# Optimization experiments

Measured on AMD Instinct MI355X. Metric: run time of the kernel, lower is better.

## Reference

```python
import jax, jax.numpy as jnp
import numpy as np

NUM_HEADS = 16
EMBED_DIM = 1024
HEAD_DIM = EMBED_DIM // NUM_HEADS


def _rel_shift(r):
    # r: (B, tlen, rlen). Pad with ONES (faithful to original), shift, tril.
    B, tlen, rlen = r.shape
    pad = jnp.ones((B, tlen, 1), dtype=r.dtype)
    rp = jnp.concatenate([pad, r], axis=2).reshape(B, rlen + 1, tlen)
    return jnp.tril(rp[:, 1:, :].reshape(B, tlen, rlen))


def setup_inputs() -> dict:
    key = jax.random.key(0)
    ks = jax.random.split(key, 12)
    T, B, E, H, D = 128, 8, EMBED_DIM, NUM_HEADS, HEAD_DIM
    query = jax.random.normal(ks[0], (T, B, E), dtype=jnp.float32)
    key_t = jax.random.normal(ks[1], (T, B, E), dtype=jnp.float32)
    value = jax.random.normal(ks[2], (T, B, E), dtype=jnp.float32)
    rel_pe = jax.random.normal(ks[3], (T, B, E), dtype=jnp.float32)
    # causal mask: True = masked (future positions)
    causal = ~jnp.tril(jnp.ones((T, T), dtype=bool))
    attn_mask = jnp.broadcast_to(causal, (B * H, T, T))
    utt_mask = jnp.ones((B * H, T, T, 1), dtype=jnp.float32)
    spk_mask = jax.random.randint(ks[4], (B, T, T), 0, 2, dtype=jnp.int32)
    s = 1.0 / np.sqrt(E)
    q_w = jax.random.uniform(ks[5], (E, E), jnp.float32, -s, s)
    k_w = jax.random.uniform(ks[6], (E, E), jnp.float32, -s, s)
    v_w = jax.random.uniform(ks[7], (E, E), jnp.float32, -s, s)
    r_w = jax.random.uniform(ks[8], (E, E), jnp.float32, -s, s)
    spk_emb = jax.random.uniform(ks[9], (2, E), jnp.float32, -s, s)
    out_w = jax.random.uniform(ks[10], (E, E), jnp.float32, -s, s)
    return {"query": query, "key": key_t, "value": value, "rel_pe": rel_pe,
            "attn_mask": attn_mask, "utt_mask": utt_mask, "spk_mask": spk_mask,
            "q_w": q_w, "k_w": k_w, "v_w": v_w, "r_w": r_w,
            "spk_emb": spk_emb, "out_w": out_w}


def reference(query, key, value, rel_pe, attn_mask, utt_mask, spk_mask,
              q_w, k_w, v_w, r_w, spk_emb, out_w):
    T, B, E = query.shape
    H, D = NUM_HEADS, HEAD_DIM
    scaling = float(D) ** -0.5

    def split_heads(x):  # (T, B, E) -> (B*H, T, D)
        return x.reshape(T, B * H, D).transpose(1, 0, 2)

    # NOTE: original computes k and v from `query` (faithful)
    q = split_heads(query @ q_w.T)
    k = split_heads(query @ k_w.T)
    v = split_heads(query @ v_w.T)
    r = split_heads(rel_pe @ r_w.T)

    # s_q: speaker embedding row 0 broadcast to all positions
    s_q = split_heads(jnp.broadcast_to(spk_emb[0], (T, B, E)))
    # s_k: (B, T, T, E) -> (B*H, T, T, D), same reshape chain as original
    s_k = spk_emb[spk_mask]                                   # (B, T, T, E)
    s_k = s_k.reshape(B, T * T, E).transpose(1, 0, 2)         # (T*T, B, E)
    s_k = s_k.reshape(T * T, B * H, D).transpose(1, 0, 2)     # (B*H, T*T, D)
    s_k = s_k.reshape(B * H, T, T, D) * utt_mask              # (B*H, T, T, D)

    new_q = q + s_q
    a1 = jnp.einsum('nid,njd->nij', new_q, k)
    a2 = jnp.einsum('nid,nijd->nij', new_q, s_k)
    a3 = _rel_shift(jnp.einsum('nid,njd->nij', s_q, r))

    w = (a1 + a2 + a3) * scaling
    w = jnp.where(attn_mask, jnp.asarray(1e-30, w.dtype), w)
    w = jax.nn.softmax(w, axis=-1)

    out = jnp.einsum('nij,njd->nid', w, v)                    # (B*H, T, D)
    out = out.transpose(1, 0, 2).reshape(T, B, E) @ out_w.T
    return out
```

## Files before the change

### kernel.cpp

```cpp
#include <hip/hip_runtime.h>
#include <hip/hip_bf16.h>
#include <cstddef>
#include <cstdint>


typedef _Float16 f16;
typedef __attribute__((ext_vector_type(8))) _Float16 f16x8;
typedef __attribute__((ext_vector_type(4))) float f32x4;

#define GLOBAL_TO_LDS(g, l) __builtin_amdgcn_global_load_lds( \
    (const __attribute__((address_space(1))) void*)(g),       \
    (__attribute__((address_space(3))) void*)(l), 16, 0, 0)

#define PIPE_SYNC(N) do {                                      \
    asm volatile("s_waitcnt vmcnt(" #N ")" ::: "memory");      \
    __builtin_amdgcn_s_barrier();                              \
    __builtin_amdgcn_sched_barrier(0);                         \
} while (0)

struct Ptr7 { const float* s[7]; };

__global__ __launch_bounds__(256) void tof16_kernel(Ptr7 p, f16* dbase)
{
    const float* s = p.s[blockIdx.y];
    f16* d = dbase + (size_t)blockIdx.y * (1u << 20);
    const int i = (blockIdx.x * 256 + threadIdx.x) * 8;
    const float4 a = *(const float4*)(s + i);
    const float4 b = *(const float4*)(s + i + 4);
    f16x8 o;
    o[0] = (f16)a.x; o[1] = (f16)a.y; o[2] = (f16)a.z; o[3] = (f16)a.w;
    o[4] = (f16)b.x; o[5] = (f16)b.y; o[6] = (f16)b.z; o[7] = (f16)b.w;
    *(f16x8*)(d + i) = o;
}

template <int TM, int TN>
__device__ __forceinline__ void gemm3ph_acc(const f16* __restrict__ A,
                                            const f16* __restrict__ B,
                                            int m0, int n0,
                                            f32x4 (&acc)[TM / 32][TN / 32])
{
    constexpr int AITS = TM / 32, BITS = TN / 32;
    constexpr int LD = AITS + BITS;
    constexpr int FM = TM / 32, FN = TN / 32;
    __shared__ __attribute__((aligned(16))) f16 As0[TM * 64];
    __shared__ __attribute__((aligned(16))) f16 As1[TM * 64];
    __shared__ __attribute__((aligned(16))) f16 As2[TM * 64];
    __shared__ __attribute__((aligned(16))) f16 Bs0[TN * 64];
    __shared__ __attribute__((aligned(16))) f16 Bs1[TN * 64];
    __shared__ __attribute__((aligned(16))) f16 Bs2[TN * 64];
    const int tid = threadIdx.x;
    const int wave = tid >> 6, lane = tid & 63;
    const int wr = wave >> 1, wc = wave & 1;
    const int l16 = lane & 15, lk = lane >> 4;

    auto stage = [&](f16* as_, f16* bs_, int k0) {
#pragma unroll
        for (int it = 0; it < AITS; ++it) {
            const int ebase = it * 2048 + wave * 512;
            const int e = ebase + lane * 8;
            const int row = e >> 6, slot = (e >> 3) & 7;
            const int scol = (slot ^ (row & 7)) << 3;
            GLOBAL_TO_LDS(A + (size_t)(m0 + row) * 1024 + k0 + scol, as_ + ebase);
        }
#pragma unroll
        for (int it = 0; it < BITS; ++it) {
            const int ebase = it * 2048 + wave * 512;
            const int e = ebase + lane * 8;
            const int row = e >> 6, slot = (e >> 3) & 7;
            const int scol = (slot ^ (row & 7)) << 3;
            GLOBAL_TO_LDS(B + (size_t)(n0 + row) * 1024 + k0 + scol, bs_ + ebase);
        }
    };
    auto compute = [&](const f16* as_, const f16* bs_) {
#pragma unroll
        for (int ksl = 0; ksl < 2; ++ksl) {
            const int s = ksl * 4 + lk;
            f16x8 af[FM], bg[FN];
#pragma unroll
            for (int mi = 0; mi < FM; ++mi) {
                const int r = wr * (TM / 2) + mi * 16 + l16;
                af[mi] = *(const f16x8*)(as_ + r * 64 + ((s ^ (r & 7)) << 3));
            }
#pragma unroll
            for (int ni = 0; ni < FN; ++ni) {
                const int r = wc * (TN / 2) + ni * 16 + l16;
                bg[ni] = *(const f16x8*)(bs_ + r * 64 + ((s ^ (r & 7)) << 3));
            }
            __builtin_amdgcn_s_setprio(1);
#pragma unroll
            for (int mi = 0; mi < FM; ++mi)
#pragma unroll
                for (int ni = 0; ni < FN; ++ni)
                    acc[mi][ni] = __builtin_amdgcn_mfma_f32_16x16x32_f16(
                        af[mi], bg[ni], acc[mi][ni], 0, 0, 0);
            __builtin_amdgcn_s_setprio(0);
        }
    };
    auto sync_steady = [&]() {
        if constexpr (LD == 6) PIPE_SYNC(6);
        else if constexpr (LD == 5) PIPE_SYNC(5);
        else PIPE_SYNC(4);
    };

    stage(As0, Bs0, 0);
    stage(As1, Bs1, 64);
    int k = 0;
#pragma unroll 1
    for (int t = 0; t < 15; t += 3) {
        sync_steady();
        if (t + 2 < 16) stage(As2, Bs2, k + 128);
        compute(As0, Bs0);
        sync_steady();
        if (t + 3 < 16) stage(As0, Bs0, k + 192);
        compute(As1, Bs1);
        sync_steady();
        if (t + 4 < 16) stage(As1, Bs1, k + 256);
        compute(As2, Bs2);
        k += 192;
    }
    PIPE_SYNC(0);
    compute(As0, Bs0);
}

__global__ __launch_bounds__(256) void proj4_kernel(
    const f16* __restrict__ qf, const f16* __restrict__ rf,
    const f16* __restrict__ wbase, const float* __restrict__ spk_emb,
    f16* __restrict__ Qh, f16* __restrict__ Kh, f16* __restrict__ VhT,
    float* __restrict__ CB, float* __restrict__ DD)
{
    const int bid = blockIdx.x;
    const int z = (bid & 7) >> 1;
    const int w = ((bid >> 3) << 1) | (bid & 1);
    const int m0 = (w >> 3) << 6;
    const int n0 = (w & 7) << 7;
    const f16* A = (z == 3) ? rf : qf;
    const f16* W = wbase + ((size_t)z << 20);

    f32x4 acc[2][4] = {};
    gemm3ph_acc<64, 128>(A, W, m0, n0, acc);

    const int tid = threadIdx.x;
    const int wave = tid >> 6, lane = tid & 63;
    const int wr = wave >> 1, wc = wave & 1;
    const int l16 = lane & 15, lk = lane >> 4;
    const int h = (n0 >> 6) + wc;

    if (z == 0) {
        float s0v[4], s1v[4];
#pragma unroll
        for (int ni = 0; ni < 4; ++ni) {
            const int c = (h << 6) + ni * 16 + l16;
            s0v[ni] = spk_emb[c];
            s1v[ni] = spk_emb[1024 + c];
        }
#pragma unroll
        for (int mi = 0; mi < 2; ++mi)
#pragma unroll
            for (int r = 0; r < 4; ++r) {
                const int row = m0 + wr * 32 + mi * 16 + lk * 4 + r;
                const int b = row & 7, t = row >> 3;
                float p0 = 0.f, p1 = 0.f;
#pragma unroll
                for (int ni = 0; ni < 4; ++ni) {
                    const float x = acc[mi][ni][r] + s0v[ni];
                    const int d = ni * 16 + l16;
                    Qh[(size_t)(((b << 4) + h) * 128 + t) * 64 + d] = (f16)x;
                    p0 = fmaf(x, s0v[ni], p0);
                    p1 = fmaf(x, s1v[ni], p1);
                }
#pragma unroll
                for (int off = 1; off < 16; off <<= 1) {
                    p0 += __shfl_xor(p0, off, 64);
                    p1 += __shfl_xor(p1, off, 64);
                }
                if (l16 == 0) {
                    const int n = (b << 4) + h;
                    DD[n * 128 + t] = p0;
                    DD[16384 + n * 128 + t] = p1;
                }
            }
    } else if (z == 3) {
        float s0v[4];
#pragma unroll
        for (int ni = 0; ni < 4; ++ni)
            s0v[ni] = spk_emb[(h << 6) + ni * 16 + l16];
#pragma unroll
        for (int mi = 0; mi < 2; ++mi)
#pragma unroll
            for (int r = 0; r < 4; ++r) {
                const int row = m0 + wr * 32 + mi * 16 + lk * 4 + r;
                const int b = row & 7, j = row >> 3;
                float p = 0.f;
#pragma unroll
                for (int ni = 0; ni < 4; ++ni)
                    p = fmaf(acc[mi][ni][r], s0v[ni], p);
#pragma unroll
                for (int off = 1; off < 16; off <<= 1)
                    p += __shfl_xor(p, off, 64);
                if (l16 == 0)
                    CB[((b << 4) + h) * 128 + j] = p;
            }
    } else {
        f16* dst = (z == 1) ? Kh : VhT;
#pragma unroll
        for (int mi = 0; mi < 2; ++mi)
#pragma unroll
            for (int r = 0; r < 4; ++r) {
                const int row = m0 + wr * 32 + mi * 16 + lk * 4 + r;
                const int b = row & 7, t = row >> 3;
#pragma unroll
                for (int ni = 0; ni < 4; ++ni) {
                    const int d = ni * 16 + l16;
                    const f16 x = (f16)acc[mi][ni][r];
                    if (z == 1)
                        dst[(size_t)(((b << 4) + h) * 128 + t) * 64 + d] = x;
                    else
                        dst[(size_t)(((b << 4) + h) * 64 + d) * 128 + t] = x;
                }
            }
    }
}

__global__ __launch_bounds__(256) void out_kernel(
    const f16* __restrict__ ATT, const f16* __restrict__ owf,
    float* __restrict__ out)
{
    const int bid = blockIdx.x;
    const int m0 = (bid >> 4) << 6;
    const int n0 = (bid & 15) << 6;
    f32x4 acc[2][2] = {};
    gemm3ph_acc<64, 64>(ATT, owf, m0, n0, acc);
    const int tid = threadIdx.x;
    const int wave = tid >> 6, lane = tid & 63;
    const int wr = wave >> 1, wc = wave & 1;
    const int l16 = lane & 15, lk = lane >> 4;
#pragma unroll
    for (int mi = 0; mi < 2; ++mi)
#pragma unroll
        for (int ni = 0; ni < 2; ++ni)
#pragma unroll
            for (int r = 0; r < 4; ++r) {
                const int row = m0 + wr * 32 + mi * 16 + lk * 4 + r;
                const int col = n0 + wc * 32 + ni * 16 + l16;
                out[(size_t)row * 1024 + col] = acc[mi][ni][r];
            }
}

__global__ __launch_bounds__(256) void attn_mfma_kernel(
    const f16* __restrict__ Qh, const f16* __restrict__ Kh,
    const f16* __restrict__ VhT,
    const float* __restrict__ CB, const float* __restrict__ DD,
    const int* __restrict__ spk_mask, const float* __restrict__ utt_mask,
    f16* __restrict__ ATT)
{
    __shared__ __attribute__((aligned(16))) char smem[58368];
    f16* nq = (f16*)smem;
    f16* kt = (f16*)(smem + 8192);
    f16* vt = (f16*)(smem + 24576);
    f16* psb = (f16*)(smem + 40960);
    float* cbuf = (float*)(smem + 57344);
    float* ddl  = (float*)(smem + 57856);

    const int bx = blockIdx.x, n = bx >> 1, half = bx & 1;
    const int b = n >> 4, h = n & 15, i0 = half << 6;
    const int tid = threadIdx.x, wave = tid >> 6, lane = tid & 63;
    const int l16 = lane & 15, lk = lane >> 4;
    const int il0 = wave * 16 + lk * 4;
    const size_t hb = (size_t)n * (128 * 64);

#pragma unroll
    for (int it = 0; it < 2; ++it) {
        const int ebase = it * 2048 + wave * 512;
        const int e = ebase + lane * 8;
        const int row = e >> 6, slot = (e >> 3) & 7;
        const int scol = (slot ^ (row & 7)) << 3;
        GLOBAL_TO_LDS(Qh + hb + (size_t)(i0 + row) * 64 + scol, nq + ebase);
    }
#pragma unroll
    for (int it = 0; it < 4; ++it) {
        const int ebase = it * 2048 + wave * 512;
        const int e = ebase + lane * 8;
        const int row = e >> 6, slot = (e >> 3) & 7;
        const int scol = (slot ^ (row & 7)) << 3;
        GLOBAL_TO_LDS(Kh + hb + (size_t)row * 64 + scol, kt + ebase);
    }
#pragma unroll
    for (int it = 0; it < 4; ++it) {
        const int ebase = it * 2048 + wave * 512;
        const int e = ebase + lane * 8;
        const int row = e >> 7, slot = (e >> 3) & 15;
        const int scol = (slot ^ (row & 7)) << 3;
        GLOBAL_TO_LDS(VhT + hb + (size_t)row * 128 + scol, vt + ebase);
    }

    if (tid < 128) {
        cbuf[tid] = CB[n * 128 + tid];
    } else {
        const int t2 = tid - 128;
        ddl[t2] = DD[(t2 >> 6) * 16384 + n * 128 + i0 + (t2 & 63)];
    }

    float du[8][4];
    int   sm[8][4];
#pragma unroll
    for (int ni = 0; ni < 8; ++ni) {
        const int j = ni * 16 + l16;
#pragma unroll
        for (int r = 0; r < 4; ++r) {
            const int i = i0 + il0 + r;
            du[ni][r] = utt_mask[((size_t)n * 128 + i) * 128 + j];
            sm[ni][r] = spk_mask[((size_t)b * 128 + i) * 128 + j];
        }
    }
    __syncthreads();

    const int iw = wave * 16 + l16;
    f16x8 af[2];
#pragma unroll
    for (int ksl = 0; ksl < 2; ++ksl) {
        const int s = ksl * 4 + lk;
        af[ksl] = *(const f16x8*)(nq + iw * 64 + ((s ^ (iw & 7)) << 3));
    }
    f32x4 sacc[8] = {};
#pragma unroll
    for (int ksl = 0; ksl < 2; ++ksl) {
        const int s = ksl * 4 + lk;
#pragma unroll
        for (int ni = 0; ni < 8; ++ni) {
            const int j = ni * 16 + l16;
            const f16x8 bg = *(const f16x8*)(kt + j * 64 + ((s ^ (j & 7)) << 3));
            sacc[ni] = __builtin_amdgcn_mfma_f32_16x16x32_f16(af[ksl], bg, sacc[ni], 0, 0, 0);
        }
    }

    float sc[8][4];
#pragma unroll
    for (int ni = 0; ni < 8; ++ni) {
        const int j = ni * 16 + l16;
#pragma unroll
        for (int r = 0; r < 4; ++r) {
            const int il = il0 + r, i = i0 + il;
            const float a2 = du[ni][r] * (sm[ni][r] ? ddl[64 + il] : ddl[il]);
            const float a3 = (j <= i) ? cbuf[127 - i + j] : 0.f;
            const float v = (sacc[ni][r] + a2 + a3) * 0.125f;
            sc[ni][r] = (j > i) ? 1e-30f : v;
        }
    }
    float inv[4];
    f16* ps = psb + wave * 2048;
#pragma unroll
    for (int r = 0; r < 4; ++r) {
        float m = sc[0][r];
#pragma unroll
        for (int ni = 1; ni < 8; ++ni) m = fmaxf(m, sc[ni][r]);
#pragma unroll
        for (int off = 8; off > 0; off >>= 1) m = fmaxf(m, __shfl_xor(m, off, 64));
        float ssum = 0.f;
#pragma unroll
        for (int ni = 0; ni < 8; ++ni) {
            const float e = __expf(sc[ni][r] - m);
            sc[ni][r] = e;
            ssum += e;
        }
#pragma unroll
        for (int off = 8; off > 0; off >>= 1) ssum += __shfl_xor(ssum, off, 64);
        inv[r] = 1.f / ssum;
    }
#pragma unroll
    for (int ni = 0; ni < 8; ++ni) {
        const int j = ni * 16 + l16;
#pragma unroll
        for (int r = 0; r < 4; ++r) {
            const int il = lk * 4 + r;
            ps[il * 128 + ((((j >> 3) ^ (il & 7)) << 3) | (j & 7))] = (f16)sc[ni][r];
        }
    }

    f16x8 pa[4];
#pragma unroll
    for (int ks = 0; ks < 4; ++ks) {
        const int slot = ks * 4 + lk;
        pa[ks] = *(const f16x8*)(ps + l16 * 128 + ((slot ^ (l16 & 7)) << 3));
    }
    f32x4 oacc[4] = {};
#pragma unroll
    for (int ks = 0; ks < 4; ++ks) {
        const int slot = ks * 4 + lk;
#pragma unroll
        for (int nd = 0; nd < 4; ++nd) {
            const int d = nd * 16 + l16;
            const f16x8 vb = *(const f16x8*)(vt + d * 128 + ((slot ^ (d & 7)) << 3));
            oacc[nd] = __builtin_amdgcn_mfma_f32_16x16x32_f16(pa[ks], vb, oacc[nd], 0, 0, 0);
        }
    }
#pragma unroll
    for (int nd = 0; nd < 4; ++nd)
#pragma unroll
        for (int r = 0; r < 4; ++r) {
            const int i = i0 + il0 + r;
            const int col = (h << 6) + nd * 16 + l16;
            ATT[(size_t)(i * 8 + b) * 1024 + col] = (f16)(oacc[nd][r] * inv[r]);
        }
}

extern "C" void kernel_launch(void* const* d_in, const int* in_sizes, int n_in,
                              void* d_out, int out_size, void* d_ws, size_t ws_size,
                              hipStream_t stream)
{
    (void)in_sizes; (void)n_in; (void)out_size; (void)ws_size;

    const float* query  = (const float*)d_in[0];
    const float* rel_pe = (const float*)d_in[3];
    const float* utt    = (const float*)d_in[5];
    const int*   spk    = (const int*)d_in[6];
    const float* qw     = (const float*)d_in[7];
    const float* kw     = (const float*)d_in[8];
    const float* vw     = (const float*)d_in[9];
    const float* rw     = (const float*)d_in[10];
    const float* spke   = (const float*)d_in[11];
    const float* ow     = (const float*)d_in[12];

    char* ws = (char*)d_ws;
    f16* Qh   = (f16*)(ws);
    f16* Kh   = (f16*)(ws + (2u  << 20));
    f16* VhT  = (f16*)(ws + (4u  << 20));
    f16* ATT  = (f16*)(ws + (6u  << 20));
    float* CB = (float*)(ws + (8u  << 20));
    float* DD = (float*)(ws + (8u << 20) + (256u << 10));
    f16* fb   = (f16*)(ws + (10u << 20));

    f16* qf = fb;
    f16* rf = fb + (1u << 20);
    f16* wb = fb + (2u << 20);
    f16* ob = fb + (6u << 20);

    Ptr7 p7;
    p7.s[0] = query; p7.s[1] = rel_pe; p7.s[2] = qw; p7.s[3] = kw;
    p7.s[4] = vw; p7.s[5] = rw; p7.s[6] = ow;

    tof16_kernel<<<dim3(512, 7), 256, 0, stream>>>(p7, fb);
    proj4_kernel<<<dim3(512), 256, 0, stream>>>(qf, rf, wb, spke, Qh, Kh, VhT, CB, DD);
    attn_mfma_kernel<<<dim3(256), 256, 0, stream>>>(Qh, Kh, VhT, CB, DD, spk, utt, ATT);
    out_kernel<<<dim3(256), 256, 0, stream>>>(ATT, ob, (float*)d_out);
}
```

Measured before the change: 48.86 us.

## Split-K the projection GEMM and add a separate reduce/epilogue kernel

The four-way projection GEMM now splits K in two, launching 1024 blocks instead of 512. Each block writes fp16 partial sums to a workspace, and a new reduce kernel adds the partials and applies the head-split, speaker-embedding and dot-product epilogues. The aim is more parallelism and better occupancy on the many-CU GPU. The cost is an extra launch, about 16 MB of extra partial-sum traffic, and fp16 rounding of the partials before they are summed.

Result: slower. 52.51 us (+7.5%).

```diff
diff --git a/kernel.cpp b/kernel.cpp
--- a/kernel.cpp
+++ b/kernel.cpp
@@ -33,15 +33,17 @@
     *(f16x8*)(d + i) = o;
 }
 
-template <int TM, int TN>
+template <int TM, int TN, int NT>
 __device__ __forceinline__ void gemm3ph_acc(const f16* __restrict__ A,
                                             const f16* __restrict__ B,
-                                            int m0, int n0,
+                                            int kbeg, int m0, int n0,
                                             f32x4 (&acc)[TM / 32][TN / 32])
 {
     constexpr int AITS = TM / 32, BITS = TN / 32;
     constexpr int LD = AITS + BITS;
     constexpr int FM = TM / 32, FN = TN / 32;
+    constexpr int T3 = (NT - 1) / 3;
+    constexpr int REM = NT - 3 * T3;
     __shared__ __attribute__((aligned(16))) f16 As0[TM * 64];
     __shared__ __attribute__((aligned(16))) f16 As1[TM * 64];
     __shared__ __attribute__((aligned(16))) f16 As2[TM * 64];
@@ -102,122 +104,132 @@
         else PIPE_SYNC(4);
     };
 
-    stage(As0, Bs0, 0);
-    stage(As1, Bs1, 64);
-    int k = 0;
+    stage(As0, Bs0, kbeg);
+    stage(As1, Bs1, kbeg + 64);
+    int k = kbeg;
 #pragma unroll 1
-    for (int t = 0; t < 15; t += 3) {
+    for (int t = 0; t < 3 * T3; t += 3) {
         sync_steady();
-        if (t + 2 < 16) stage(As2, Bs2, k + 128);
+        if (t + 2 < NT) stage(As2, Bs2, k + 128);
         compute(As0, Bs0);
         sync_steady();
-        if (t + 3 < 16) stage(As0, Bs0, k + 192);
+        if (t + 3 < NT) stage(As0, Bs0, k + 192);
         compute(As1, Bs1);
         sync_steady();
-        if (t + 4 < 16) stage(As1, Bs1, k + 256);
+        if (t + 4 < NT) stage(As1, Bs1, k + 256);
         compute(As2, Bs2);
         k += 192;
     }
-    PIPE_SYNC(0);
-    compute(As0, Bs0);
+    if constexpr (REM == 2) {
+        sync_steady();
+        compute(As0, Bs0);
+        PIPE_SYNC(0);
+        compute(As1, Bs1);
+    } else {
+        PIPE_SYNC(0);
+        compute(As0, Bs0);
+    }
 }
 
 __global__ __launch_bounds__(256) void proj4_kernel(
     const f16* __restrict__ qf, const f16* __restrict__ rf,
-    const f16* __restrict__ wbase, const float* __restrict__ spk_emb,
-    f16* __restrict__ Qh, f16* __restrict__ Kh, f16* __restrict__ VhT,
-    float* __restrict__ CB, float* __restrict__ DD)
+    const f16* __restrict__ wbase, f16* __restrict__ Pp)
 {
     const int bid = blockIdx.x;
     const int z = (bid & 7) >> 1;
-    const int w = ((bid >> 3) << 1) | (bid & 1);
-    const int m0 = (w >> 3) << 6;
-    const int n0 = (w & 7) << 7;
+    const int w2 = ((bid >> 3) << 1) | (bid & 1);
+    const int tile = w2 >> 1;
+    const int kz = w2 & 1;
+    const int m0 = (tile >> 3) << 6;
+    const int n0 = (tile & 7) << 7;
     const f16* A = (z == 3) ? rf : qf;
     const f16* W = wbase + ((size_t)z << 20);
 
     f32x4 acc[2][4] = {};
-    gemm3ph_acc<64, 128>(A, W, m0, n0, acc);
-
+    gemm3ph_acc<64, 128, 8>(A, W, kz * 512, m0, n0, acc);
+
+    f16* P = Pp + ((size_t)(z * 2 + kz) << 20);
     const int tid = threadIdx.x;
     const int wave = tid >> 6, lane = tid & 63;
     const int wr = wave >> 1, wc = wave & 1;
     const int l16 = lane & 15, lk = lane >> 4;
-    const int h = (n0 >> 6) + wc;
-
-    if (z == 0) {
-        float s0v[4], s1v[4];
-#pragma unroll
-        for (int ni = 0; ni < 4; ++ni) {
-            const int c = (h << 6) + ni * 16 + l16;
-            s0v[ni] = spk_emb[c];
-            s1v[ni] = spk_emb[1024 + c];
-        }
-#pragma unroll
-        for (int mi = 0; mi < 2; ++mi)
+#pragma unroll
+    for (int mi = 0; mi < 2; ++mi)
+#pragma unroll
+        for (int ni = 0; ni < 4; ++ni)
 #pragma unroll
             for (int r = 0; r < 4; ++r) {
                 const int row = m0 + wr * 32 + mi * 16 + lk * 4 + r;
-                const int b = row & 7, t = row >> 3;
-                float p0 = 0.f, p1 = 0.f;
-#pragma unroll
-                for (int ni = 0; ni < 4; ++ni) {
-                    const float x = acc[mi][ni][r] + s0v[ni];
-                    const int d = ni * 16 + l16;
-                    Qh[(size_t)(((b << 4) + h) * 128 + t) * 64 + d] = (f16)x;
-                    p0 = fmaf(x, s0v[ni], p0);
-                    p1 = fmaf(x, s1v[ni], p1);
-                }
-#pragma unroll
-                for (int off = 1; off < 16; off <<= 1) {
-                    p0 += __shfl_xor(p0, off, 64);
-                    p1 += __shfl_xor(p1, off, 64);
-                }
-                if (l16 == 0) {
-                    const int n = (b << 4) + h;
-                    DD[n * 128 + t] = p0;
-                    DD[16384 + n * 128 + t] = p1;
-                }
+                const int col = n0 + wc * 64 + ni * 16 + l16;
+                P[(size_t)row * 1024 + col] = (f16)acc[mi][ni][r];
             }
-    } else if (z == 3) {
-        float s0v[4];
-#pragma unroll
-        for (int ni = 0; ni < 4; ++ni)
-            s0v[ni] = spk_emb[(h << 6) + ni * 16 + l16];
-#pragma unroll
-        for (int mi = 0; mi < 2; ++mi)
-#pragma unroll
-            for (int r = 0; r < 4; ++r) {
-                const int row = m0 + wr * 32 + mi * 16 + lk * 4 + r;
-                const int b = row & 7, j = row >> 3;
-                float p = 0.f;
-#pragma unroll
-                for (int ni = 0; ni < 4; ++ni)
-                    p = fmaf(acc[mi][ni][r], s0v[ni], p);
-#pragma unroll
-                for (int off = 1; off < 16; off <<= 1)
-                    p += __shfl_xor(p, off, 64);
-                if (l16 == 0)
-                    CB[((b << 4) + h) * 128 + j] = p;
-            }
+}
+
+__global__ __launch_bounds__(256) void reduce_kernel(
+    const f16* __restrict__ Pp, const float* __restrict__ spk_emb,
+    f16* __restrict__ Qh, f16* __restrict__ Kh, f16* __restrict__ VhT,
+    float* __restrict__ CB, float* __restrict__ DD)
+{
+    const int z = blockIdx.y;
+    const int bb = blockIdx.x;
+    const int rb = bb >> 3, cb = bb & 7;
+    const int t = threadIdx.x;
+    const int row = rb * 16 + (t >> 4);
+    const int col = cb * 128 + (t & 15) * 8;
+
+    const f16* P0 = Pp + ((size_t)(z * 2 + 0) << 20);
+    const f16* P1 = Pp + ((size_t)(z * 2 + 1) << 20);
+    const f16x8 a = *(const f16x8*)(P0 + (size_t)row * 1024 + col);
+    const f16x8 b = *(const f16x8*)(P1 + (size_t)row * 1024 + col);
+    float xs[8];
+#pragma unroll
+    for (int j = 0; j < 8; ++j) xs[j] = (float)a[j] + (float)b[j];
+
+    const int h = col >> 6, d0 = col & 63;
+    const int brow = row & 7, trow = row >> 3;
+    const int n = (brow << 4) + h;
+
+    if (z == 0) {
+        float p0 = 0.f, p1 = 0.f;
+        f16x8 o;
+#pragma unroll
+        for (int j = 0; j < 8; ++j) {
+            const float s0 = spk_emb[h * 64 + d0 + j];
+            const float s1 = spk_emb[1024 + h * 64 + d0 + j];
+            const float nq = xs[j] + s0;
+            o[j] = (f16)nq;
+            p0 = fmaf(nq, s0, p0);
+            p1 = fmaf(nq, s1, p1);
+        }
+        *(f16x8*)(Qh + ((size_t)n * 128 + trow) * 64 + d0) = o;
+#pragma unroll
+        for (int off = 1; off < 8; off <<= 1) {
+            p0 += __shfl_xor(p0, off, 64);
+            p1 += __shfl_xor(p1, off, 64);
+        }
+        if ((t & 7) == 0) {
+            DD[n * 128 + trow] = p0;
+            DD[16384 + n * 128 + trow] = p1;
+        }
+    } else if (z == 1) {
+        f16x8 o;
+#pragma unroll
+        for (int j = 0; j < 8; ++j) o[j] = (f16)xs[j];
+        *(f16x8*)(Kh + ((size_t)n * 128 + trow) * 64 + d0) = o;
+    } else if (z == 2) {
+#pragma unroll
+        for (int j = 0; j < 8; ++j)
+            VhT[((size_t)n * 64 + d0 + j) * 128 + trow] = (f16)xs[j];
     } else {
-        f16* dst = (z == 1) ? Kh : VhT;
-#pragma unroll
-        for (int mi = 0; mi < 2; ++mi)
-#pragma unroll
-            for (int r = 0; r < 4; ++r) {
-                const int row = m0 + wr * 32 + mi * 16 + lk * 4 + r;
-                const int b = row & 7, t = row >> 3;
-#pragma unroll
-                for (int ni = 0; ni < 4; ++ni) {
-                    const int d = ni * 16 + l16;
-                    const f16 x = (f16)acc[mi][ni][r];
-                    if (z == 1)
-                        dst[(size_t)(((b << 4) + h) * 128 + t) * 64 + d] = x;
-                    else
-                        dst[(size_t)(((b << 4) + h) * 64 + d) * 128 + t] = x;
-                }
-            }
+        float p = 0.f;
+#pragma unroll
+        for (int j = 0; j < 8; ++j)
+            p = fmaf(xs[j], spk_emb[h * 64 + d0 + j], p);
+#pragma unroll
+        for (int off = 1; off < 8; off <<= 1)
+            p += __shfl_xor(p, off, 64);
+        if ((t & 7) == 0)
+            CB[n * 128 + trow] = p;
     }
 }
 
@@ -229,7 +241,7 @@
     const int m0 = (bid >> 4) << 6;
     const int n0 = (bid & 15) << 6;
     f32x4 acc[2][2] = {};
-    gemm3ph_acc<64, 64>(ATT, owf, m0, n0, acc);
+    gemm3ph_acc<64, 64, 16>(ATT, owf, 0, m0, n0, acc);
     const int tid = threadIdx.x;
     const int wave = tid >> 6, lane = tid & 63;
     const int wr = wave >> 1, wc = wave & 1;
@@ -428,6 +440,7 @@
     float* CB = (float*)(ws + (8u  << 20));
     float* DD = (float*)(ws + (8u << 20) + (256u << 10));
     f16* fb   = (f16*)(ws + (10u << 20));
+    f16* Pp   = (f16*)(ws + (24u << 20));
 
     f16* qf = fb;
     f16* rf = fb + (1u << 20);
@@ -439,7 +452,8 @@
     p7.s[4] = vw; p7.s[5] = rw; p7.s[6] = ow;
 
     tof16_kernel<<<dim3(512, 7), 256, 0, stream>>>(p7, fb);
-    proj4_kernel<<<dim3(512), 256, 0, stream>>>(qf, rf, wb, spke, Qh, Kh, VhT, CB, DD);
+    proj4_kernel<<<dim3(1024), 256, 0, stream>>>(qf, rf, wb, Pp);
+    reduce_kernel<<<dim3(512, 4), 256, 0, stream>>>(Pp, spke, Qh, Kh, VhT, CB, DD);
     attn_mfma_kernel<<<dim3(256), 256, 0, stream>>>(Qh, Kh, VhT, CB, DD, spk, utt, ATT);
     out_kernel<<<dim3(256), 256, 0, stream>>>(ATT, ob, (float*)d_out);
 }
```

## Fuse fp32-to-fp16 conversion into projection GEMM via register-staged pipeline

Applied to the files above, without the earlier changes.

The projection kernel now reads fp32 query/rel_pe and weights directly, converts them to fp16 in registers, and writes swizzled tiles into a triple-buffered LDS pipeline. The previous pass that converted six of the seven inputs to fp16 is removed, so only out_w is still converted separately. This drops a full read/write round trip for about 6M elements and one launch. The cost is twice the global read bytes inside the GEMM and register-staged loads in place of async global-to-LDS copies. The generic GEMM helper also gains K-range/tile-count parameters.

Result: slower. 56.67 us (+16.0%).

```diff
diff --git a/kernel.cpp b/kernel.cpp
--- a/kernel.cpp
+++ b/kernel.cpp
@@ -18,12 +18,15 @@
     __builtin_amdgcn_sched_barrier(0);                         \
 } while (0)
 
-struct Ptr7 { const float* s[7]; };
-
-__global__ __launch_bounds__(256) void tof16_kernel(Ptr7 p, f16* dbase)
+#define LBAR() do {                                            \
+    asm volatile("s_waitcnt lgkmcnt(0)" ::: "memory");         \
+    __builtin_amdgcn_s_barrier();                              \
+    __builtin_amdgcn_sched_barrier(0);                         \
+} while (0)
+
+__global__ __launch_bounds__(256) void tof16ow_kernel(const float* __restrict__ s,
+                                                      f16* __restrict__ d)
 {
-    const float* s = p.s[blockIdx.y];
-    f16* d = dbase + (size_t)blockIdx.y * (1u << 20);
     const int i = (blockIdx.x * 256 + threadIdx.x) * 8;
     const float4 a = *(const float4*)(s + i);
     const float4 b = *(const float4*)(s + i + 4);
@@ -33,15 +36,17 @@
     *(f16x8*)(d + i) = o;
 }
 
-template <int TM, int TN>
+template <int TM, int TN, int NT>
 __device__ __forceinline__ void gemm3ph_acc(const f16* __restrict__ A,
                                             const f16* __restrict__ B,
-                                            int m0, int n0,
+                                            int kbeg, int m0, int n0,
                                             f32x4 (&acc)[TM / 32][TN / 32])
 {
     constexpr int AITS = TM / 32, BITS = TN / 32;
     constexpr int LD = AITS + BITS;
     constexpr int FM = TM / 32, FN = TN / 32;
+    constexpr int T3 = (NT - 1) / 3;
+    constexpr int REM = NT - 3 * T3;
     __shared__ __attribute__((aligned(16))) f16 As0[TM * 64];
     __shared__ __attribute__((aligned(16))) f16 As1[TM * 64];
     __shared__ __attribute__((aligned(16))) f16 As2[TM * 64];
@@ -102,49 +107,149 @@
         else PIPE_SYNC(4);
     };
 
-    stage(As0, Bs0, 0);
-    stage(As1, Bs1, 64);
-    int k = 0;
+    stage(As0, Bs0, kbeg);
+    stage(As1, Bs1, kbeg + 64);
+    int k = kbeg;
 #pragma unroll 1
-    for (int t = 0; t < 15; t += 3) {
+    for (int t = 0; t < 3 * T3; t += 3) {
         sync_steady();
-        if (t + 2 < 16) stage(As2, Bs2, k + 128);
+        if (t + 2 < NT) stage(As2, Bs2, k + 128);
         compute(As0, Bs0);
         sync_steady();
-        if (t + 3 < 16) stage(As0, Bs0, k + 192);
+        if (t + 3 < NT) stage(As0, Bs0, k + 192);
         compute(As1, Bs1);
         sync_steady();
-        if (t + 4 < 16) stage(As1, Bs1, k + 256);
+        if (t + 4 < NT) stage(As1, Bs1, k + 256);
         compute(As2, Bs2);
         k += 192;
     }
-    PIPE_SYNC(0);
-    compute(As0, Bs0);
+    if constexpr (REM == 2) {
+        sync_steady();
+        compute(As0, Bs0);
+        PIPE_SYNC(0);
+        compute(As1, Bs1);
+    } else {
+        PIPE_SYNC(0);
+        compute(As0, Bs0);
+    }
 }
 
-__global__ __launch_bounds__(256) void proj4_kernel(
-    const f16* __restrict__ qf, const f16* __restrict__ rf,
-    const f16* __restrict__ wbase, const float* __restrict__ spk_emb,
+__global__ __launch_bounds__(256, 2) void proj4rs_kernel(
+    const float* __restrict__ query, const float* __restrict__ rel_pe,
+    const float* __restrict__ qw, const float* __restrict__ kw,
+    const float* __restrict__ vw, const float* __restrict__ rw,
+    const float* __restrict__ spk_emb,
     f16* __restrict__ Qh, f16* __restrict__ Kh, f16* __restrict__ VhT,
     float* __restrict__ CB, float* __restrict__ DD)
 {
+    __shared__ __attribute__((aligned(16))) f16 As0[64 * 64];
+    __shared__ __attribute__((aligned(16))) f16 As1[64 * 64];
+    __shared__ __attribute__((aligned(16))) f16 As2[64 * 64];
+    __shared__ __attribute__((aligned(16))) f16 Bs0[128 * 64];
+    __shared__ __attribute__((aligned(16))) f16 Bs1[128 * 64];
+    __shared__ __attribute__((aligned(16))) f16 Bs2[128 * 64];
+
     const int bid = blockIdx.x;
     const int z = (bid & 7) >> 1;
     const int w = ((bid >> 3) << 1) | (bid & 1);
     const int m0 = (w >> 3) << 6;
     const int n0 = (w & 7) << 7;
-    const f16* A = (z == 3) ? rf : qf;
-    const f16* W = wbase + ((size_t)z << 20);
-
-    f32x4 acc[2][4] = {};
-    gemm3ph_acc<64, 128>(A, W, m0, n0, acc);
+    const float* A = (z == 3) ? rel_pe : query;
+    const float* W = (z == 0) ? qw : (z == 1) ? kw : (z == 2) ? vw : rw;
 
     const int tid = threadIdx.x;
     const int wave = tid >> 6, lane = tid & 63;
     const int wr = wave >> 1, wc = wave & 1;
     const int l16 = lane & 15, lk = lane >> 4;
+
+    float4 ra[2][2], rb[4][2];
+    f32x4 acc[2][4] = {};
+
+    auto load_stage = [&](int k0) {
+#pragma unroll
+        for (int it = 0; it < 2; ++it) {
+            const int e = it * 2048 + wave * 512 + lane * 8;
+            const int row = e >> 6, slot = (e >> 3) & 7;
+            const float* s = A + (size_t)(m0 + row) * 1024 + k0 + slot * 8;
+            ra[it][0] = *(const float4*)s;
+            ra[it][1] = *(const float4*)(s + 4);
+        }
+#pragma unroll
+        for (int it = 0; it < 4; ++it) {
+            const int e = it * 2048 + wave * 512 + lane * 8;
+            const int row = e >> 6, slot = (e >> 3) & 7;
+            const float* s = W + (size_t)(n0 + row) * 1024 + k0 + slot * 8;
+            rb[it][0] = *(const float4*)s;
+            rb[it][1] = *(const float4*)(s + 4);
+        }
+    };
+    auto write_stage = [&](f16* as_, f16* bs_) {
+#pragma unroll
+        for (int it = 0; it < 2; ++it) {
+            const int e = it * 2048 + wave * 512 + lane * 8;
+            const int row = e >> 6, slot = (e >> 3) & 7;
+            f16x8 o;
+            o[0] = (f16)ra[it][0].x; o[1] = (f16)ra[it][0].y;
+            o[2] = (f16)ra[it][0].z; o[3] = (f16)ra[it][0].w;
+            o[4] = (f16)ra[it][1].x; o[5] = (f16)ra[it][1].y;
+            o[6] = (f16)ra[it][1].z; o[7] = (f16)ra[it][1].w;
+            *(f16x8*)(as_ + row * 64 + ((slot ^ (row & 7)) << 3)) = o;
+        }
+#pragma unroll
+        for (int it = 0; it < 4; ++it) {
+            const int e = it * 2048 + wave * 512 + lane * 8;
+            const int row = e >> 6, slot = (e >> 3) & 7;
+            f16x8 o;
+            o[0] = (f16)rb[it][0].x; o[1] = (f16)rb[it][0].y;
+            o[2] = (f16)rb[it][0].z; o[3] = (f16)rb[it][0].w;
+            o[4] = (f16)rb[it][1].x; o[5] = (f16)rb[it][1].y;
+            o[6] = (f16)rb[it][1].z; o[7] = (f16)rb[it][1].w;
+            *(f16x8*)(bs_ + row * 64 + ((slot ^ (row & 7)) << 3)) = o;
+        }
+    };
+    auto compute = [&](const f16* as_, const f16* bs_) {
+#pragma unroll
+        for (int ksl = 0; ksl < 2; ++ksl) {
+            const int s = ksl * 4 + lk;
+            f16x8 af[2], bg[4];
+#pragma unroll
+            for (int mi = 0; mi < 2; ++mi) {
+                const int r = wr * 32 + mi * 16 + l16;
+                af[mi] = *(const f16x8*)(as_ + r * 64 + ((s ^ (r & 7)) << 3));
+            }
+#pragma unroll
+            for (int ni = 0; ni < 4; ++ni) {
+                const int r = wc * 64 + ni * 16 + l16;
+                bg[ni] = *(const f16x8*)(bs_ + r * 64 + ((s ^ (r & 7)) << 3));
+            }
+            __builtin_amdgcn_s_setprio(1);
+#pragma unroll
+            for (int mi = 0; mi < 2; ++mi)
+#pragma unroll
+                for (int ni = 0; ni < 4; ++ni)
+                    acc[mi][ni] = __builtin_amdgcn_mfma_f32_16x16x32_f16(
+                        af[mi], bg[ni], acc[mi][ni], 0, 0, 0);
+            __builtin_amdgcn_s_setprio(0);
+        }
+    };
+
+    f16* Asb[3] = {As0, As1, As2};
+    f16* Bsb[3] = {Bs0, Bs1, Bs2};
+
+    load_stage(0);
+    write_stage(As0, Bs0);
+    load_stage(64);
+    LBAR();
+
+#pragma unroll
+    for (int t = 0; t < 16; ++t) {
+        if (t + 1 < 16) write_stage(Asb[(t + 1) % 3], Bsb[(t + 1) % 3]);
+        if (t + 2 < 16) load_stage((t + 2) * 64);
+        compute(Asb[t % 3], Bsb[t % 3]);
+        LBAR();
+    }
+
     const int h = (n0 >> 6) + wc;
-
     if (z == 0) {
         float s0v[4], s1v[4];
 #pragma unroll
@@ -229,7 +334,7 @@
     const int m0 = (bid >> 4) << 6;
     const int n0 = (bid & 15) << 6;
     f32x4 acc[2][2] = {};
-    gemm3ph_acc<64, 64>(ATT, owf, m0, n0, acc);
+    gemm3ph_acc<64, 64, 16>(ATT, owf, 0, m0, n0, acc);
     const int tid = threadIdx.x;
     const int wave = tid >> 6, lane = tid & 63;
     const int wr = wave >> 1, wc = wave & 1;
@@ -427,19 +532,11 @@
     f16* ATT  = (f16*)(ws + (6u  << 20));
     float* CB = (float*)(ws + (8u  << 20));
     float* DD = (float*)(ws + (8u << 20) + (256u << 10));
-    f16* fb   = (f16*)(ws + (10u << 20));
-
-    f16* qf = fb;
-    f16* rf = fb + (1u << 20);
-    f16* wb = fb + (2u << 20);
-    f16* ob = fb + (6u << 20);
-
-    Ptr7 p7;
-    p7.s[0] = query; p7.s[1] = rel_pe; p7.s[2] = qw; p7.s[3] = kw;
-    p7.s[4] = vw; p7.s[5] = rw; p7.s[6] = ow;
-
-    tof16_kernel<<<dim3(512, 7), 256, 0, stream>>>(p7, fb);
-    proj4_kernel<<<dim3(512), 256, 0, stream>>>(qf, rf, wb, spke, Qh, Kh, VhT, CB, DD);
+    f16* ob   = (f16*)(ws + (10u << 20));
+
+    tof16ow_kernel<<<dim3(512), 256, 0, stream>>>(ow, ob);
+    proj4rs_kernel<<<dim3(512), 256, 0, stream>>>(query, rel_pe, qw, kw, vw, rw,
+                                                  spke, Qh, Kh, VhT, CB, DD);
     attn_mfma_kernel<<<dim3(256), 256, 0, stream>>>(Qh, Kh, VhT, CB, DD, spk, utt, ATT);
     out_kernel<<<dim3(256), 256, 0, stream>>>(ATT, ob, (float*)d_out);
 }
```
